# Performance work log

Measured on AMD Instinct MI355X. Metric: run time of the kernel, lower is better.

The kernel has to match this reference:

```python
import jax, jax.numpy as jnp
import numpy as np

# Keyed conv layer as structured SpMM in affine coordinates.
# W (N x N sparse, N = C*H*W + 1) stored in ELL format: for each output row r,
# cols[r, :] are the K column indices and vals[r, :] the nonzero values.
C, H, W_, KS = 32, 32, 32, 3
N = C * H * W_ + 1          # 32769, homogeneous (+1 bias) dim
K = C * KS * KS             # 288 nnz per row (Toeplitz conv structure)
B = 32                      # batch


def setup_inputs() -> dict:
    key = jax.random.key(0)
    k1, k2, k3 = jax.random.split(key, 3)
    x_affine = jax.random.normal(k1, (B, N), dtype=jnp.float32)
    cols = jax.random.randint(k2, (N, K), 0, N, dtype=jnp.int32)
    vals = jax.random.normal(k3, (N, K), dtype=jnp.float32) / np.float32(np.sqrt(K))
    return {"x_affine": x_affine, "vals": vals, "cols": cols}


def reference(x_affine, vals, cols):
    # y = (W @ x_affine^T)^T  with W in row-wise ELL format.
    # Gather input features addressed by each row's nonzero columns, then
    # contract over the K nonzeros of each row.
    xg = x_affine[:, cols]                      # [B, N, K] gathered features
    y = jnp.einsum('bnk,nk->bn', xg, vals)      # [B, N]
    return y
```

## Files before the change

### kernel.cpp

```cpp
#include <hip/hip_runtime.h>

constexpr int B = 32;
constexpr int N = 32 * 32 * 32 + 1;
constexpr int K = 32 * 3 * 3;

using i4 = __attribute__((ext_vector_type(4))) int;
using f4 = __attribute__((ext_vector_type(4))) float;
using h4 = __attribute__((ext_vector_type(4))) _Float16;

__global__ __launch_bounds__(256) void transpose_x_f16_kernel(
    const float* __restrict__ x, _Float16* __restrict__ xT) {
  __shared__ float tile[32][33];
  const int n0 = blockIdx.x * 32;
  const int t  = threadIdx.x;
  const int lb = t & 31;
  const int lr = t >> 5;
#pragma unroll
  for (int i = 0; i < 4; ++i) {
    const int b = lr + i * 8;
    const int n = n0 + lb;
    float v = 0.f;
    if (n < N) v = x[(size_t)b * N + n];
    tile[lb][b] = v;
  }
  __syncthreads();
#pragma unroll
  for (int i = 0; i < 4; ++i) {
    const int nl = lr + i * 8;
    const int n  = n0 + nl;
    if (n < N) xT[(size_t)n * B + lb] = (_Float16)tile[nl][lb];
  }
}

__global__ __launch_bounds__(256, 4) void gather_dot_f16_kernel(
    const _Float16* __restrict__ xT, const float* __restrict__ vals,
    const int* __restrict__ cols, float* __restrict__ yT) {
  __shared__ int scols[32 * K];
  const int t    = threadIdx.x;
  const int lane = t & 63;
  const int wave = t >> 6;
  const int g    = lane >> 3;
  const int bq   = lane & 7;
  const int n0   = blockIdx.x * 32;

  constexpr int SLAB_BYTES = 32 * K * 4;
  constexpr int ROUNDS     = SLAB_BYTES / 4096;
  const char* slab = (const char*)(cols + (size_t)n0 * K);
  const long long avail = ((long long)N * K - (long long)n0 * K) * 4;
#pragma unroll
  for (int r = 0; r < ROUNDS; ++r) {
    const int off  = r * 4096 + t * 16;
    const int goff = (off + 16 <= avail) ? off : 0;
    __builtin_amdgcn_global_load_lds(
        (const __attribute__((address_space(1))) void*)(slab + goff),
        (__attribute__((address_space(3))) void*)((char*)scols + off),
        16, 0, 0);
  }
  __syncthreads();

  const int nl = wave * 8 + g;
  const int n  = n0 + nl;
  if (n >= N) return;

  const int*   __restrict__ srow = scols + nl * K;
  const float* __restrict__ vrow = vals + (size_t)n * K;

  f4 acc0 = {0.f, 0.f, 0.f, 0.f};
  f4 acc1 = {0.f, 0.f, 0.f, 0.f};

  const int rot = g * 8;

#pragma unroll 4
  for (int k = 0; k < K; k += 8) {
    int kk = k + rot;
    if (kk >= K) kk -= K;

    const i4 c0 = *reinterpret_cast<const i4*>(srow + kk);
    const i4 c1 = *reinterpret_cast<const i4*>(srow + kk + 4);
    const f4 v0 = *reinterpret_cast<const f4*>(vrow + kk);
    const f4 v1 = *reinterpret_cast<const f4*>(vrow + kk + 4);

    const h4 x0 = *reinterpret_cast<const h4*>(xT + (size_t)c0.x * B + bq * 4);
    const h4 x1 = *reinterpret_cast<const h4*>(xT + (size_t)c0.y * B + bq * 4);
    const h4 x2 = *reinterpret_cast<const h4*>(xT + (size_t)c0.z * B + bq * 4);
    const h4 x3 = *reinterpret_cast<const h4*>(xT + (size_t)c0.w * B + bq * 4);
    const h4 x4 = *reinterpret_cast<const h4*>(xT + (size_t)c1.x * B + bq * 4);
    const h4 x5 = *reinterpret_cast<const h4*>(xT + (size_t)c1.y * B + bq * 4);
    const h4 x6 = *reinterpret_cast<const h4*>(xT + (size_t)c1.z * B + bq * 4);
    const h4 x7 = *reinterpret_cast<const h4*>(xT + (size_t)c1.w * B + bq * 4);

    acc0 += __builtin_convertvector(x0, f4) * v0.x;
    acc0 += __builtin_convertvector(x1, f4) * v0.y;
    acc0 += __builtin_convertvector(x2, f4) * v0.z;
    acc0 += __builtin_convertvector(x3, f4) * v0.w;
    acc1 += __builtin_convertvector(x4, f4) * v1.x;
    acc1 += __builtin_convertvector(x5, f4) * v1.y;
    acc1 += __builtin_convertvector(x6, f4) * v1.z;
    acc1 += __builtin_convertvector(x7, f4) * v1.w;
  }

  acc0 += acc1;
  *reinterpret_cast<f4*>(yT + (size_t)n * B + bq * 4) = acc0;
}

__global__ __launch_bounds__(256) void transpose_y_kernel(
    const float* __restrict__ yT, float* __restrict__ y) {
  __shared__ float tile[32][33];
  const int n0 = blockIdx.x * 32;
  const int t  = threadIdx.x;
  const int lb = t & 31;
  const int lr = t >> 5;
#pragma unroll
  for (int i = 0; i < 4; ++i) {
    const int nl = lr + i * 8;
    const int n  = n0 + nl;
    float v = 0.f;
    if (n < N) v = yT[(size_t)n * B + lb];
    tile[nl][lb] = v;
  }
  __syncthreads();
#pragma unroll
  for (int i = 0; i < 4; ++i) {
    const int b = lr + i * 8;
    const int n = n0 + lb;
    if (n < N) y[(size_t)b * N + n] = tile[lb][b];
  }
}

__global__ __launch_bounds__(256) void gather_dot_fallback(
    const float* __restrict__ x, const float* __restrict__ vals,
    const int* __restrict__ cols, float* __restrict__ y) {
  const int t    = threadIdx.x;
  const int lane = t & 63;
  const int wave = t >> 6;
  const int g    = lane >> 3;
  const int bq   = lane & 7;
  const int n    = blockIdx.x * 32 + wave * 8 + g;
  if (n >= N) return;
  const int*   crow = cols + (size_t)n * K;
  const float* vrow = vals + (size_t)n * K;
  float4 acc = make_float4(0.f, 0.f, 0.f, 0.f);
  for (int k = 0; k < K; ++k) {
    const int   c = crow[k];
    const float v = vrow[k];
    acc.x += x[(size_t)(bq * 4 + 0) * N + c] * v;
    acc.y += x[(size_t)(bq * 4 + 1) * N + c] * v;
    acc.z += x[(size_t)(bq * 4 + 2) * N + c] * v;
    acc.w += x[(size_t)(bq * 4 + 3) * N + c] * v;
  }
  y[(size_t)(bq * 4 + 0) * N + n] = acc.x;
  y[(size_t)(bq * 4 + 1) * N + n] = acc.y;
  y[(size_t)(bq * 4 + 2) * N + n] = acc.z;
  y[(size_t)(bq * 4 + 3) * N + n] = acc.w;
}

extern "C" void kernel_launch(void* const* d_in, const int* in_sizes, int n_in,
                              void* d_out, int out_size, void* d_ws, size_t ws_size,
                              hipStream_t stream) {
  const float* x    = (const float*)d_in[0];
  const float* vals = (const float*)d_in[1];
  const int*   cols = (const int*)d_in[2];
  float*       y    = (float*)d_out;

  const size_t nb       = (size_t)N * B;
  const size_t xT_bytes = nb * sizeof(_Float16);
  const size_t need     = xT_bytes + nb * sizeof(float);

  const int nblocks = (N + 31) / 32;

  if (ws_size >= need) {
    _Float16* xT = (_Float16*)d_ws;
    float*    yT = (float*)((char*)d_ws + xT_bytes);
    transpose_x_f16_kernel<<<nblocks, 256, 0, stream>>>(x, xT);
    gather_dot_f16_kernel<<<nblocks, 256, 0, stream>>>(xT, vals, cols, yT);
    transpose_y_kernel<<<nblocks, 256, 0, stream>>>(yT, y);
  } else {
    gather_dot_fallback<<<nblocks, 256, 0, stream>>>(x, vals, cols, y);
  }
}
```

Measured before the change: 174.1 us.

## Pack column indices to 16-bit in LDS and raise occupancy of the gather kernel

Each block now loads its column-index slab with ordinary vector loads, packs each index to 16 bits, and stores the result in shared memory. This halves the LDS footprint per block, which allows the launch bound to rise from 4 to 8 blocks per unit. In the inner loop, one 16-byte LDS read supplies eight indices, and each byte offset into the transposed fp16 x is built with a 32-bit shift and mask instead of 64-bit index arithmetic. The trade-off is that the async global-to-LDS copy becomes a synchronous register path, and the packing assumes N is at most 65536.

Result: no change. 173.4 us (-0.4%).

```diff
diff --git a/kernel.cpp b/kernel.cpp
--- a/kernel.cpp
+++ b/kernel.cpp
@@ -32,10 +32,10 @@
   }
 }
 
-__global__ __launch_bounds__(256, 4) void gather_dot_f16_kernel(
+__global__ __launch_bounds__(256, 8) void gather_dot_f16_u16_kernel(
     const _Float16* __restrict__ xT, const float* __restrict__ vals,
     const int* __restrict__ cols, float* __restrict__ yT) {
-  __shared__ int scols[32 * K];
+  __shared__ unsigned short scols[32 * K];
   const int t    = threadIdx.x;
   const int lane = t & 63;
   const int wave = t >> 6;
@@ -43,18 +43,20 @@
   const int bq   = lane & 7;
   const int n0   = blockIdx.x * 32;
 
-  constexpr int SLAB_BYTES = 32 * K * 4;
-  constexpr int ROUNDS     = SLAB_BYTES / 4096;
-  const char* slab = (const char*)(cols + (size_t)n0 * K);
-  const long long avail = ((long long)N * K - (long long)n0 * K) * 4;
+  {
+    const long long last = (long long)N * K - 4;
+    unsigned int* sc32 = (unsigned int*)scols;
 #pragma unroll
-  for (int r = 0; r < ROUNDS; ++r) {
-    const int off  = r * 4096 + t * 16;
-    const int goff = (off + 16 <= avail) ? off : 0;
-    __builtin_amdgcn_global_load_lds(
-        (const __attribute__((address_space(1))) void*)(slab + goff),
-        (__attribute__((address_space(3))) void*)((char*)scols + off),
-        16, 0, 0);
+    for (int r = 0; r < 9; ++r) {
+      const int c = r * 256 + t;
+      long long gi = (long long)n0 * K + (long long)c * 4;
+      if (gi > last) gi = last;
+      const i4 w = *reinterpret_cast<const i4*>(cols + gi);
+      const unsigned int p0 = (unsigned int)(w.x & 0xFFFF) | ((unsigned int)w.y << 16);
+      const unsigned int p1 = (unsigned int)(w.z & 0xFFFF) | ((unsigned int)w.w << 16);
+      sc32[c * 2]     = p0;
+      sc32[c * 2 + 1] = p1;
+    }
   }
   __syncthreads();
 
@@ -62,8 +64,9 @@
   const int n  = n0 + nl;
   if (n >= N) return;
 
-  const int*   __restrict__ srow = scols + nl * K;
-  const float* __restrict__ vrow = vals + (size_t)n * K;
+  const unsigned short* __restrict__ srow = scols + nl * K;
+  const char* __restrict__ xTb  = (const char*)xT + bq * 8;
+  const char* __restrict__ vrow = (const char*)(vals + (size_t)n * K);
 
   f4 acc0 = {0.f, 0.f, 0.f, 0.f};
   f4 acc1 = {0.f, 0.f, 0.f, 0.f};
@@ -75,19 +78,31 @@
     int kk = k + rot;
     if (kk >= K) kk -= K;
 
-    const i4 c0 = *reinterpret_cast<const i4*>(srow + kk);
-    const i4 c1 = *reinterpret_cast<const i4*>(srow + kk + 4);
-    const f4 v0 = *reinterpret_cast<const f4*>(vrow + kk);
-    const f4 v1 = *reinterpret_cast<const f4*>(vrow + kk + 4);
+    const i4 cp = *reinterpret_cast<const i4*>(srow + kk);
+    const f4 v0 = *reinterpret_cast<const f4*>(vrow + kk * 4);
+    const f4 v1 = *reinterpret_cast<const f4*>(vrow + kk * 4 + 16);
 
-    const h4 x0 = *reinterpret_cast<const h4*>(xT + (size_t)c0.x * B + bq * 4);
-    const h4 x1 = *reinterpret_cast<const h4*>(xT + (size_t)c0.y * B + bq * 4);
-    const h4 x2 = *reinterpret_cast<const h4*>(xT + (size_t)c0.z * B + bq * 4);
-    const h4 x3 = *reinterpret_cast<const h4*>(xT + (size_t)c0.w * B + bq * 4);
-    const h4 x4 = *reinterpret_cast<const h4*>(xT + (size_t)c1.x * B + bq * 4);
-    const h4 x5 = *reinterpret_cast<const h4*>(xT + (size_t)c1.y * B + bq * 4);
-    const h4 x6 = *reinterpret_cast<const h4*>(xT + (size_t)c1.z * B + bq * 4);
-    const h4 x7 = *reinterpret_cast<const h4*>(xT + (size_t)c1.w * B + bq * 4);
+    const unsigned int w0 = (unsigned int)cp.x;
+    const unsigned int w1 = (unsigned int)cp.y;
+    const unsigned int w2 = (unsigned int)cp.z;
+    const unsigned int w3 = (unsigned int)cp.w;
+    const unsigned int o0 = (w0 << 6) & 0x3FFFC0u;
+    const unsigned int o1 = (w0 >> 10) & 0x3FFFC0u;
+    const unsigned int o2 = (w1 << 6) & 0x3FFFC0u;
+    const unsigned int o3 = (w1 >> 10) & 0x3FFFC0u;
+    const unsigned int o4 = (w2 << 6) & 0x3FFFC0u;
+    const unsigned int o5 = (w2 >> 10) & 0x3FFFC0u;
+    const unsigned int o6 = (w3 << 6) & 0x3FFFC0u;
+    const unsigned int o7 = (w3 >> 10) & 0x3FFFC0u;
+
+    const h4 x0 = *reinterpret_cast<const h4*>(xTb + o0);
+    const h4 x1 = *reinterpret_cast<const h4*>(xTb + o1);
+    const h4 x2 = *reinterpret_cast<const h4*>(xTb + o2);
+    const h4 x3 = *reinterpret_cast<const h4*>(xTb + o3);
+    const h4 x4 = *reinterpret_cast<const h4*>(xTb + o4);
+    const h4 x5 = *reinterpret_cast<const h4*>(xTb + o5);
+    const h4 x6 = *reinterpret_cast<const h4*>(xTb + o6);
+    const h4 x7 = *reinterpret_cast<const h4*>(xTb + o7);
 
     acc0 += __builtin_convertvector(x0, f4) * v0.x;
     acc0 += __builtin_convertvector(x1, f4) * v0.y;
@@ -172,7 +187,7 @@
     _Float16* xT = (_Float16*)d_ws;
     float*    yT = (float*)((char*)d_ws + xT_bytes);
     transpose_x_f16_kernel<<<nblocks, 256, 0, stream>>>(x, xT);
-    gather_dot_f16_kernel<<<nblocks, 256, 0, stream>>>(xT, vals, cols, yT);
+    gather_dot_f16_u16_kernel<<<nblocks, 256, 0, stream>>>(xT, vals, cols, yT);
     transpose_y_kernel<<<nblocks, 256, 0, stream>>>(yT, y);
   } else {
     gather_dot_fallback<<<nblocks, 256, 0, stream>>>(x, vals, cols, y);
```
